# Kernel optimization log

Measured on AMD Instinct MI355X. Metric: run time of the kernel, lower is better.

The kernel has to match this reference:

```python
import jax, jax.numpy as jnp
import numpy as np

NUM_HEADS = 12
HEAD_SIZE = 64
HIDDEN = NUM_HEADS * HEAD_SIZE  # 768
ONE_SIDED_WINDOW = 256          # attention_window 512 // 2
NEG = -10000.0


def setup_inputs() -> dict:
    key = jax.random.key(0)
    ks = jax.random.split(key, 16)
    B, W, E, H = 1, 2048, 128, HIDDEN
    std = 0.02
    def lin(kw, kb):
        return (jax.random.normal(kw, (H, H), jnp.float32) * std,
                jax.random.normal(kb, (H,), jnp.float32) * std)
    q_w, q_b = lin(ks[0], ks[1])
    k_w, k_b = lin(ks[2], ks[3])
    v_w, v_b = lin(ks[4], ks[5])
    w2e_w, w2e_b = lin(ks[6], ks[7])
    e2w_w, e2w_b = lin(ks[8], ks[9])
    e2e_w, e2e_b = lin(ks[10], ks[11])
    return {
        "word_hidden_states": jax.random.normal(ks[12], (B, W, H), jnp.float32),
        "entity_hidden_states": jax.random.normal(ks[13], (B, E, H), jnp.float32),
        "attention_mask": jnp.zeros((B, 1, 1, W + E), jnp.float32),
        "q_w": q_w, "q_b": q_b, "k_w": k_w, "k_b": k_b, "v_w": v_w, "v_b": v_b,
        "w2e_w": w2e_w, "w2e_b": w2e_b, "e2w_w": e2w_w, "e2w_b": e2w_b,
        "e2e_w": e2e_w, "e2e_b": e2e_b,
    }


def reference(word_hidden_states, entity_hidden_states, attention_mask,
              q_w, q_b, k_w, k_b, v_w, v_b,
              w2e_w, w2e_b, e2w_w, e2w_b, e2e_w, e2e_b):
    B, W, H = word_hidden_states.shape
    E = entity_hidden_states.shape[1]
    S = W + E

    def heads(x):  # [B, L, H] -> [B, nh, L, hd]
        return x.reshape(B, -1, NUM_HEADS, HEAD_SIZE).transpose(0, 2, 1, 3)

    concat = jnp.concatenate([word_hidden_states, entity_hidden_states], axis=1)
    k = heads(concat @ k_w + k_b)          # [B, nh, S, hd]
    v = heads(concat @ v_w + v_b)
    q_w2w = heads(word_hidden_states @ q_w + q_b)
    q_w2e = heads(word_hidden_states @ w2e_w + w2e_b)
    q_e2w = heads(entity_hidden_states @ e2w_w + e2w_b)
    q_e2e = heads(entity_hidden_states @ e2e_w + e2e_b)

    k_word, k_ent = k[:, :, :W], k[:, :, W:]

    # --- w2w: Longformer sliding-window QK^T, then _conversion to a dense
    # [B, nh, W, W] matrix with out-of-band entries set to -10000. ---
    w2w = jnp.einsum('bhid,bhjd->bhij', q_w2w, k_word)  # [B, nh, W, W]
    idx = jnp.arange(W)
    in_band = jnp.abs(idx[:, None] - idx[None, :]) <= ONE_SIDED_WINDOW  # [W, W]
    # diagonal mask: float_mask[j] (-10000 where attention_mask != 0) added
    # within the band (broadcast over heads / query positions)
    mask_words = attention_mask[:, 0, 0, :W]                # [B, W]
    float_mask = jnp.where(mask_words != 0.0, NEG, 0.0)     # [B, W]
    w2w = w2w + float_mask[:, None, None, :]
    # _conversion: out-of-band -> -10000; also exact zeros -> -10000 (source quirk)
    w2w = jnp.where(in_band[None, None] & (w2w != 0.0), w2w, NEG)

    # --- entity-aware dense blocks ---
    w2e = jnp.einsum('bhid,bhjd->bhij', q_w2e, k_ent)    # [B, nh, W, E]
    e2w = jnp.einsum('bhid,bhjd->bhij', q_e2w, k_word)   # [B, nh, E, W]
    e2e = jnp.einsum('bhid,bhjd->bhij', q_e2e, k_ent)    # [B, nh, E, E]

    word_scores = jnp.concatenate([w2w, w2e], axis=3)    # [B, nh, W, S]
    ent_scores = jnp.concatenate([e2w, e2e], axis=3)     # [B, nh, E, S]
    scores = jnp.concatenate([word_scores, ent_scores], axis=2)  # [B, nh, S, S]

    scores = scores / jnp.sqrt(jnp.float32(HEAD_SIZE)) + attention_mask
    probs = jax.nn.softmax(scores, axis=-1)

    ctx = jnp.einsum('bhij,bhjd->bhid', probs, v)        # [B, nh, S, hd]
    ctx = ctx.transpose(0, 2, 1, 3).reshape(B, S, H)
    return ctx[:, :W, :], ctx[:, W:, :]
```

## Files before the change

kernel.cpp:

```cpp
#include <hip/hip_runtime.h>

typedef __bf16 bf16x8 __attribute__((ext_vector_type(8)));
typedef unsigned short u16x8 __attribute__((ext_vector_type(8)));
typedef u16x8 u16x8_a __attribute__((may_alias));
typedef unsigned int u32x2 __attribute__((ext_vector_type(2)));
typedef u32x2 u32x2_a __attribute__((may_alias));
typedef unsigned int u32x4 __attribute__((ext_vector_type(4)));
typedef u32x4 u32x4_a __attribute__((may_alias));
typedef float f32x4 __attribute__((ext_vector_type(4)));
typedef float f32x16 __attribute__((ext_vector_type(16)));

#define LOG2E 1.4426950408889634f
#define NEGV  -10000.0f

__device__ __forceinline__ unsigned int cvtpk(float lo, float hi){
  unsigned int r;
  asm("v_cvt_pk_bf16_f32 %0, %1, %2" : "=v"(r) : "v"(lo), "v"(hi));
  return r;
}
__device__ __forceinline__ bf16x8 ldb(const unsigned short* p){
  return __builtin_bit_cast(bf16x8, *(const u16x8_a*)p);
}
__device__ __forceinline__ bf16x8 mkfrag(unsigned a, unsigned b, unsigned c, unsigned d){
  u32x4 v = {a,b,c,d};
  return __builtin_bit_cast(bf16x8, v);
}
__device__ __forceinline__ void gload16(const unsigned short* g, unsigned short* l){
  __builtin_amdgcn_global_load_lds(
    (const __attribute__((address_space(1))) void*)g,
    (__attribute__((address_space(3))) void*)l, 16, 0, 0);
}

__global__ __launch_bounds__(256) void prep(
    const float* __restrict__ w0, const float* __restrict__ w1,
    const float* __restrict__ w2, const float* __restrict__ w3,
    const float* __restrict__ w4, const float* __restrict__ w5,
    const float* __restrict__ word, const float* __restrict__ ent,
    const float* __restrict__ am,
    unsigned short* __restrict__ outT, unsigned short* __restrict__ Abf,
    float* __restrict__ amT, float* __restrict__ negT)
{
  int z = blockIdx.z, tid = threadIdx.x;
  if (z == 6){
    size_t id = (size_t)blockIdx.y*24 + blockIdx.x;
    size_t e = (id*256 + tid)*8;
    const size_t WE = (size_t)2048*768;
    const float* s = (e < WE) ? (word + e) : (ent + (e - WE));
    float4 a = *(const float4*)s;
    float4 b = *(const float4*)(s+4);
    u32x4 v = {cvtpk(a.x,a.y), cvtpk(a.z,a.w), cvtpk(b.x,b.y), cvtpk(b.z,b.w)};
    *(u32x4_a*)(Abf + e) = v;
    return;
  }
  if (z == 7){
    if (blockIdx.y != 0 || blockIdx.x >= 9) return;
    int j = blockIdx.x*256 + tid;
    if (j < 2176){
      float a = am[j];
      amT[j]  = a * LOG2E;
      negT[j] = (a != 0.f) ? NEGV : 0.f;
    }
    return;
  }
  if (blockIdx.y >= 24) return;
  const float* src;
  switch (z){
    case 0: src = w0; break; case 1: src = w1; break; case 2: src = w2; break;
    case 3: src = w3; break; case 4: src = w4; break; default: src = w5; break;
  }
  unsigned short* dst = outT + (size_t)z * 589824;
  __shared__ float tile[32][33];
  int tx = tid & 31, ty = tid >> 5;
  int x0 = blockIdx.x*32, y0 = blockIdx.y*32;
  #pragma unroll
  for (int i=0;i<32;i+=8) tile[ty+i][tx] = src[(size_t)(y0+ty+i)*768 + x0+tx];
  __syncthreads();
  #pragma unroll
  for (int i=0;i<32;i+=16){
    unsigned int u = cvtpk(tile[tx][ty+i], tile[tx][ty+i+8]);
    dst[(size_t)(x0+ty+i)*768 + y0+tx]   = (unsigned short)u;
    dst[(size_t)(x0+ty+i+8)*768 + y0+tx] = (unsigned short)(u>>16);
  }
}

__global__ __launch_bounds__(256) void gemm_proj(
    const unsigned short* __restrict__ Abf,
    const unsigned short* __restrict__ wT,
    const float* __restrict__ bK, const float* __restrict__ bV,
    const float* __restrict__ bQ, const float* __restrict__ bWE,
    const float* __restrict__ bEW, const float* __restrict__ bEE,
    unsigned short* __restrict__ oK, unsigned short* __restrict__ VbT,
    unsigned short* __restrict__ oQ, unsigned short* __restrict__ oWE,
    unsigned short* __restrict__ oEW, unsigned short* __restrict__ oEE)
{
  int mt = blockIdx.x, ntile = blockIdx.y;
  int g, mg;
  if      (mt < 17){ g=0; mg=mt;    }
  else if (mt < 34){ g=1; mg=mt-17; }
  else if (mt < 50){ g=2; mg=mt-34; }
  else if (mt < 66){ g=3; mg=mt-50; }
  else if (mt < 67){ g=4; mg=0;     }
  else             { g=5; mg=0;     }
  int m0 = mg*128;
  const unsigned short* A = Abf + (size_t)((g>=4 ? 2048 : 0) + m0)*768;
  const unsigned short* B = wT + (size_t)g*589824;
  const float* bias; unsigned short* out;
  switch (g){
    case 0: bias=bK;  out=oK;  break;
    case 1: bias=bV;  out=0;   break;
    case 2: bias=bQ;  out=oQ;  break;
    case 3: bias=bWE; out=oWE; break;
    case 4: bias=bEW; out=oEW; break;
    default:bias=bEE; out=oEE; break;
  }
  int n0 = ntile*128;

  __shared__ __align__(16) unsigned short a_s[128*32];
  __shared__ __align__(16) unsigned short b_s[128*32];

  int tid  = threadIdx.x;
  int w    = tid>>6, lane = tid&63, quad = lane>>4, lr = lane&15;
  int wm   = (w&1)*64, wn = (w>>1)*64;

  f32x4 acc[4][4];
  #pragma unroll
  for (int i=0;i<4;i++) for (int j=0;j<4;j++) for (int r=0;r<4;r++) acc[i][j][r]=0.f;

  int srow = lane>>2;
  int scol = (lane&3)*8;
  const unsigned short* gA0 = A + (size_t)(w*32 + srow)*768 + scol;
  const unsigned short* gA1 = gA0 + (size_t)16*768;
  const unsigned short* gB0 = B + (size_t)(n0 + w*32 + srow)*768 + scol;
  const unsigned short* gB1 = gB0 + (size_t)16*768;
  unsigned short* lA0 = a_s + w*32*32;
  unsigned short* lA1 = lA0 + 16*32;
  unsigned short* lB0 = b_s + w*32*32;
  unsigned short* lB1 = lB0 + 16*32;

  for (int k0=0; k0<768; k0+=32){
    __syncthreads();
    gload16(gA0 + k0, lA0);
    gload16(gA1 + k0, lA1);
    gload16(gB0 + k0, lB0);
    gload16(gB1 + k0, lB1);
    __syncthreads();
    bf16x8 af[4], bfr[4];
    #pragma unroll
    for (int i=0;i<4;i++) af[i]  = ldb(a_s + (wm+i*16+lr)*32 + quad*8);
    #pragma unroll
    for (int j=0;j<4;j++) bfr[j] = ldb(b_s + (wn+j*16+lr)*32 + quad*8);
    #pragma unroll
    for (int i=0;i<4;i++)
      #pragma unroll
      for (int j=0;j<4;j++)
        acc[i][j] = __builtin_amdgcn_mfma_f32_16x16x32_bf16(af[i], bfr[j], acc[i][j], 0,0,0);
  }
  if (g == 1){
    #pragma unroll
    for (int j=0;j<4;j++){
      int col = n0 + wn + j*16 + lr;
      float bb = bias[col];
      #pragma unroll
      for (int i=0;i<4;i++){
        int rowb = m0 + wm + i*16 + quad*4;
        u32x2 uv = {cvtpk(acc[i][j][0]+bb, acc[i][j][1]+bb),
                    cvtpk(acc[i][j][2]+bb, acc[i][j][3]+bb)};
        *(u32x2_a*)(VbT + (size_t)col*2176 + rowb) = uv;
      }
    }
  } else {
    out += (size_t)m0*768;
    #pragma unroll
    for (int j=0;j<4;j++){
      int col = n0 + wn + j*16 + lr;
      float bb = bias[col];
      #pragma unroll
      for (int i=0;i<4;i++){
        int rowb = wm + i*16 + quad*4;
        unsigned int u01 = cvtpk(acc[i][j][0]+bb, acc[i][j][1]+bb);
        unsigned int u23 = cvtpk(acc[i][j][2]+bb, acc[i][j][3]+bb);
        out[(size_t)(rowb+0)*768 + col] = (unsigned short)u01;
        out[(size_t)(rowb+1)*768 + col] = (unsigned short)(u01>>16);
        out[(size_t)(rowb+2)*768 + col] = (unsigned short)u23;
        out[(size_t)(rowb+3)*768 + col] = (unsigned short)(u23>>16);
      }
    }
  }
}

__global__ __launch_bounds__(256, 4) void attn_split(
  const unsigned short* __restrict__ Kb,  const unsigned short* __restrict__ VbT,
  const unsigned short* __restrict__ Qw,  const unsigned short* __restrict__ Qwe,
  const unsigned short* __restrict__ Qew, const unsigned short* __restrict__ Qee,
  const float* __restrict__ amT, const float* __restrict__ negT,
  float* __restrict__ outw, float* __restrict__ pO, float* __restrict__ pML)
{
  int lin = blockIdx.x + 80*blockIdx.y;
  int wid = (lin & 7)*120 + (lin >> 3);
  int bx = wid % 80;
  int h  = wid / 80;

  int tid = threadIdx.x, w = tid>>6, lane = tid&63;
  int l31 = lane & 31, hi = lane >> 5;
  int hi8 = hi*8, hi4 = hi*4;
  bool isword = bx < 64;
  int qrb, eg=0, eq=0;
  const unsigned short *Qa, *Qb;
  if (isword){ qrb = bx*32; Qa=Qw;  Qb=Qwe; }
  else       { int e = bx-64; eg = e>>2; eq = e&3; qrb = eg*32; Qa=Qew; Qb=Qee; }
  int hofs = h*64;

  __shared__ float part[4][64][35];

  float m = -1e30f, l = 0.f;
  f32x16 o0, o1;
  #pragma unroll
  for (int r=0;r<16;r++){ o0[r] = 0.f; o1[r] = 0.f; }

  int lo, nw, start, end;
  if (isword){
    lo = qrb - 256; if (lo < 0) lo = 0;
    int hiq = qrb + 288; if (hiq > 2048) hiq = 2048;
    nw = (hiq - lo) >> 5;
    start = w; end = nw + 4;
  } else {
    lo = 0; nw = 64;
    start = eq*17 + w; end = eq*17 + 17;
  }
  int iq = qrb + l31;
  int end1 = (nw < end) ? nw : end;
  int c1   = start + ((nw - start + 3) & ~3);

#define AITER(J0, QF0, QF1, QF2, QF3, BAND) do { \
    int j0 = (J0); \
    const unsigned short* kp = Kb + (size_t)(j0+l31)*768 + hofs + hi8; \
    bf16x8 ka0 = ldb(kp), ka1 = ldb(kp+16), ka2 = ldb(kp+32), ka3 = ldb(kp+48); \
    float4 aT0 = *(const float4*)(amT + j0 + hi4); \
    float4 aT1 = *(const float4*)(amT + j0 + 8  + hi4); \
    float4 aT2 = *(const float4*)(amT + j0 + 16 + hi4); \
    float4 aT3 = *(const float4*)(amT + j0 + 24 + hi4); \
    f32x16 s; \
    _Pragma("unroll") \
    for (int r=0;r<16;r++) s[r] = 0.f; \
    __builtin_amdgcn_s_setprio(1); \
    s = __builtin_amdgcn_mfma_f32_32x32x16_bf16(ka0, QF0, s, 0,0,0); \
    s = __builtin_amdgcn_mfma_f32_32x32x16_bf16(ka1, QF1, s, 0,0,0); \
    s = __builtin_amdgcn_mfma_f32_32x32x16_bf16(ka2, QF2, s, 0,0,0); \
    s = __builtin_amdgcn_mfma_f32_32x32x16_bf16(ka3, QF3, s, 0,0,0); \
    __builtin_amdgcn_s_setprio(0); \
    const unsigned short* vp = VbT + (size_t)(hofs + l31)*2176 + j0 + hi8; \
    bf16x8 va00 = ldb(vp),           va01 = ldb(vp + 16); \
    bf16x8 va10 = ldb(vp + 32*2176), va11 = ldb(vp + 32*2176 + 16); \
    float sc[16]; \
    if (BAND){ \
      float4 nT0 = *(const float4*)(negT + j0 + hi4); \
      float4 nT1 = *(const float4*)(negT + j0 + 8  + hi4); \
      float4 nT2 = *(const float4*)(negT + j0 + 16 + hi4); \
      float4 nT3 = *(const float4*)(negT + j0 + 24 + hi4); \
      int djb = iq + 256 - (j0 + hi4); \
      _Pragma("unroll") \
      for (int e=0;e<4;e++){ \
        { float sv = s[e]    + nT0[e]; \
          bool ok = ((unsigned)(djb - e)      <= 512u) && (sv != 0.f); \
          sc[e]    = (ok ? sv : NEGV) * (LOG2E*0.125f) + aT0[e]; } \
        { float sv = s[4+e]  + nT1[e]; \
          bool ok = ((unsigned)(djb - 8 - e)  <= 512u) && (sv != 0.f); \
          sc[4+e]  = (ok ? sv : NEGV) * (LOG2E*0.125f) + aT1[e]; } \
        { float sv = s[8+e]  + nT2[e]; \
          bool ok = ((unsigned)(djb - 16 - e) <= 512u) && (sv != 0.f); \
          sc[8+e]  = (ok ? sv : NEGV) * (LOG2E*0.125f) + aT2[e]; } \
        { float sv = s[12+e] + nT3[e]; \
          bool ok = ((unsigned)(djb - 24 - e) <= 512u) && (sv != 0.f); \
          sc[12+e] = (ok ? sv : NEGV) * (LOG2E*0.125f) + aT3[e]; } \
      } \
    } else { \
      _Pragma("unroll") \
      for (int e=0;e<4;e++){ \
        sc[e]    = s[e]    * (LOG2E*0.125f) + aT0[e]; \
        sc[4+e]  = s[4+e]  * (LOG2E*0.125f) + aT1[e]; \
        sc[8+e]  = s[8+e]  * (LOG2E*0.125f) + aT2[e]; \
        sc[12+e] = s[12+e] * (LOG2E*0.125f) + aT3[e]; \
      } \
    } \
    float mx = sc[0]; \
    _Pragma("unroll") \
    for (int r=1;r<16;r++) mx = fmaxf(mx, sc[r]); \
    mx = fmaxf(mx, __shfl_xor(mx, 32)); \
    float mn; \
    if (__all(mx <= m)){ \
      mn = m; \
    } else { \
      mn = fmaxf(m, mx); \
      float alpha = exp2f(m - mn); \
      m = mn; \
      l *= alpha; \
      _Pragma("unroll") \
      for (int r=0;r<16;r++){ o0[r] *= alpha; o1[r] *= alpha; } \
    } \
    float p[16]; \
    _Pragma("unroll") \
    for (int r=0;r<16;r++) p[r] = exp2f(sc[r]-mn); \
    float rs = ((p[0]+p[1])+(p[2]+p[3])) + ((p[4]+p[5])+(p[6]+p[7])) \
             + ((p[8]+p[9])+(p[10]+p[11])) + ((p[12]+p[13])+(p[14]+p[15])); \
    rs += __shfl_xor(rs, 32); \
    l += rs; \
    unsigned pk0 = cvtpk(p[0], p[1]),  pk1 = cvtpk(p[2], p[3]); \
    unsigned pk2 = cvtpk(p[4], p[5]),  pk3 = cvtpk(p[6], p[7]); \
    unsigned pk4 = cvtpk(p[8], p[9]),  pk5 = cvtpk(p[10], p[11]); \
    unsigned pk6 = cvtpk(p[12], p[13]),pk7 = cvtpk(p[14], p[15]); \
    bool hib = hi != 0; \
    unsigned t0 = hib ? pk0 : pk2; \
    unsigned t1 = hib ? pk1 : pk3; \
    unsigned t2 = hib ? pk4 : pk6; \
    unsigned t3 = hib ? pk5 : pk7; \
    unsigned r0 = (unsigned)__shfl_xor((int)t0, 32); \
    unsigned r1 = (unsigned)__shfl_xor((int)t1, 32); \
    unsigned r2 = (unsigned)__shfl_xor((int)t2, 32); \
    unsigned r3 = (unsigned)__shfl_xor((int)t3, 32); \
    bf16x8 pf1 = hib ? mkfrag(r0, r1, pk2, pk3) : mkfrag(pk0, pk1, r0, r1); \
    bf16x8 pf2 = hib ? mkfrag(r2, r3, pk6, pk7) : mkfrag(pk4, pk5, r2, r3); \
    __builtin_amdgcn_s_setprio(1); \
    o0 = __builtin_amdgcn_mfma_f32_32x32x16_bf16(va00, pf1, o0, 0,0,0); \
    o0 = __builtin_amdgcn_mfma_f32_32x32x16_bf16(va01, pf2, o0, 0,0,0); \
    o1 = __builtin_amdgcn_mfma_f32_32x32x16_bf16(va10, pf1, o1, 0,0,0); \
    o1 = __builtin_amdgcn_mfma_f32_32x32x16_bf16(va11, pf2, o1, 0,0,0); \
    __builtin_amdgcn_s_setprio(0); \
  } while(0)

  {
    const unsigned short* qr = Qa + (size_t)(qrb+l31)*768 + hofs + hi8;
    bf16x8 qa0 = ldb(qr), qa1 = ldb(qr+16), qa2 = ldb(qr+32), qa3 = ldb(qr+48);
    for (int c = start; c < end1; c += 4)
      AITER(lo + c*32, qa0, qa1, qa2, qa3, isword);
  }
  __builtin_amdgcn_sched_barrier(0);
  if (c1 < end){
    const unsigned short* qr = Qb + (size_t)(qrb+l31)*768 + hofs + hi8;
    bf16x8 qb0 = ldb(qr), qb1 = ldb(qr+16), qb2 = ldb(qr+32), qb3 = ldb(qr+48);
    for (int c = c1; c < end; c += 4)
      AITER(2048 + (c-nw)*32, qb0, qb1, qb2, qb3, false);
  }
#undef AITER

  {
    float* my = &part[w][lane][0];
    my[0] = m; my[1] = l;
    #pragma unroll
    for (int r=0;r<16;r++){ my[2+r] = o0[r]; my[18+r] = o1[r]; }
  }
  __syncthreads();

  float mm[4], ll[4], e4[4];
  #pragma unroll
  for (int p=0;p<4;p++){ mm[p] = part[p][lane][0]; ll[p] = part[p][lane][1]; }
  float M = fmaxf(fmaxf(mm[0],mm[1]), fmaxf(mm[2],mm[3]));
  #pragma unroll
  for (int p=0;p<4;p++) e4[p] = exp2f(mm[p]-M);
  float L = ll[0]*e4[0] + ll[1]*e4[1] + ll[2]*e4[2] + ll[3]*e4[3];

  float mo0[4], mo1[4];
  #pragma unroll
  for (int k=0;k<4;k++){
    float a0 = 0.f, a1 = 0.f;
    #pragma unroll
    for (int p=0;p<4;p++){
      a0 += part[p][lane][2  + w*4 + k] * e4[p];
      a1 += part[p][lane][18 + w*4 + k] * e4[p];
    }
    mo0[k] = a0; mo1[k] = a1;
  }

  if (isword){
    float rinv = 1.f / L;
    float4 s0 = {mo0[0]*rinv, mo0[1]*rinv, mo0[2]*rinv, mo0[3]*rinv};
    float4 s1 = {mo1[0]*rinv, mo1[1]*rinv, mo1[2]*rinv, mo1[3]*rinv};
    float* ob = outw + (size_t)(qrb+l31)*768 + hofs + w*8 + hi4;
    *(float4*)(ob)      = s0;
    *(float4*)(ob + 32) = s1;
  } else {
    int idx = (eg*4 + eq)*12 + h;
    float* po = pO + (size_t)idx*2048 + l31*64 + w*8 + hi4;
    float4 s0 = {mo0[0], mo0[1], mo0[2], mo0[3]};
    float4 s1 = {mo1[0], mo1[1], mo1[2], mo1[3]};
    *(float4*)(po)      = s0;
    *(float4*)(po + 32) = s1;
    if (w == 0 && lane < 32){
      float* pml = pML + (size_t)idx*64;
      pml[lane*2]     = M;
      pml[lane*2 + 1] = L;
    }
  }
}

__global__ __launch_bounds__(256) void merge_ent(
    const float* __restrict__ pO, const float* __restrict__ pML,
    float* __restrict__ oute)
{
  int b = blockIdx.x;
  int eg = b/12, h = b%12;
  int tid = threadIdx.x;
  int row = tid>>3, cg = (tid&7)*8;
  float mq[4], lq[4];
  #pragma unroll
  for (int q=0;q<4;q++){
    int idx = (eg*4 + q)*12 + h;
    mq[q] = pML[(size_t)idx*64 + row*2];
    lq[q] = pML[(size_t)idx*64 + row*2 + 1];
  }
  float M = fmaxf(fmaxf(mq[0],mq[1]), fmaxf(mq[2],mq[3]));
  float L = 0.f, eqv[4];
  #pragma unroll
  for (int q=0;q<4;q++){ eqv[q] = exp2f(mq[q]-M); L += lq[q]*eqv[q]; }
  float rl = 1.f/L;
  float4 a0 = {0,0,0,0}, a1 = {0,0,0,0};
  #pragma unroll
  for (int q=0;q<4;q++){
    int idx = (eg*4 + q)*12 + h;
    const float* src = pO + (size_t)idx*2048 + row*64 + cg;
    float4 x = *(const float4*)(src);
    float4 y = *(const float4*)(src + 4);
    a0.x += x.x*eqv[q]; a0.y += x.y*eqv[q]; a0.z += x.z*eqv[q]; a0.w += x.w*eqv[q];
    a1.x += y.x*eqv[q]; a1.y += y.y*eqv[q]; a1.z += y.z*eqv[q]; a1.w += y.w*eqv[q];
  }
  a0.x*=rl; a0.y*=rl; a0.z*=rl; a0.w*=rl;
  a1.x*=rl; a1.y*=rl; a1.z*=rl; a1.w*=rl;
  float* dst = oute + (size_t)(eg*32+row)*768 + h*64 + cg;
  *(float4*)(dst)   = a0;
  *(float4*)(dst+4) = a1;
}

extern "C" void kernel_launch(void* const* d_in, const int* in_sizes, int n_in,
                              void* d_out, int out_size, void* d_ws, size_t ws_size,
                              hipStream_t stream) {
  const float* word  = (const float*)d_in[0];
  const float* ent   = (const float*)d_in[1];
  const float* am    = (const float*)d_in[2];
  const float* q_w   = (const float*)d_in[3];
  const float* q_b   = (const float*)d_in[4];
  const float* k_w   = (const float*)d_in[5];
  const float* k_b   = (const float*)d_in[6];
  const float* v_w   = (const float*)d_in[7];
  const float* v_b   = (const float*)d_in[8];
  const float* w2e_w = (const float*)d_in[9];
  const float* w2e_b = (const float*)d_in[10];
  const float* e2w_w = (const float*)d_in[11];
  const float* e2w_b = (const float*)d_in[12];
  const float* e2e_w = (const float*)d_in[13];
  const float* e2e_b = (const float*)d_in[14];

  unsigned short* ws  = (unsigned short*)d_ws;
  unsigned short* wT  = ws;
  unsigned short* Kb  = wT  + (size_t)6*589824;
  unsigned short* Tb  = Kb  + (size_t)2176*768;
  unsigned short* Qw  = Tb  + (size_t)2176*768;
  unsigned short* Qwe = Qw  + (size_t)2048*768;
  unsigned short* Qew = Qwe + (size_t)2048*768;
  unsigned short* Qee = Qew + (size_t)128*768;
  unsigned short* VbT = Qee + (size_t)128*768;
  unsigned short* Abf = VbT + (size_t)768*2176;

  float* amT  = (float*)Tb;
  float* negT = amT + 2176;

  float* pO  = (float*)wT;
  float* pML = pO + (size_t)192*2048;

  float* outw = (float*)d_out;
  float* oute = outw + (size_t)2048*768;

  hipLaunchKernelGGL(prep, dim3(24,34,8), dim3(256), 0, stream,
                     k_w, v_w, q_w, w2e_w, e2w_w, e2e_w, word, ent, am,
                     wT, Abf, amT, negT);
  hipLaunchKernelGGL(gemm_proj, dim3(68,6), dim3(256), 0, stream,
                     Abf, wT, k_b, v_b, q_b, w2e_b, e2w_b, e2e_b,
                     Kb, VbT, Qw, Qwe, Qew, Qee);
  hipLaunchKernelGGL(attn_split, dim3(80,12), dim3(256), 0, stream,
                     Kb, VbT, Qw, Qwe, Qew, Qee, amT, negT, outw, pO, pML);
  hipLaunchKernelGGL(merge_ent, dim3(48), dim3(256), 0, stream,
                     pO, pML, oute);
}
```

Measured before the change: 154.2 us.

## Double-buffer K fragments in registers and relax attention kernel launch bounds

The attention loop now loads the next tile's K fragments into a second register set before it computes the current tile, alternating between two buffers. This hides global-load latency behind the MFMA and softmax work. The entity tail loop becomes a single iteration because it can run at most once, and the sched_barrier is dropped. The min-blocks-per-CU hint of 4 is removed so the compiler can use more registers for the extra buffers, at the risk of lower occupancy.

```diff
diff --git a/kernel.cpp b/kernel.cpp
--- a/kernel.cpp
+++ b/kernel.cpp
@@ -188,7 +188,7 @@
   }
 }
 
-__global__ __launch_bounds__(256, 4) void attn_split(
+__global__ __launch_bounds__(256) void attn_split(
   const unsigned short* __restrict__ Kb,  const unsigned short* __restrict__ VbT,
   const unsigned short* __restrict__ Qw,  const unsigned short* __restrict__ Qwe,
   const unsigned short* __restrict__ Qew, const unsigned short* __restrict__ Qee,
@@ -217,47 +217,45 @@
   #pragma unroll
   for (int r=0;r<16;r++){ o0[r] = 0.f; o1[r] = 0.f; }
 
-  int lo, nw, start, end;
+  int lo, b, s1, endT;
   if (isword){
     lo = qrb - 256; if (lo < 0) lo = 0;
     int hiq = qrb + 288; if (hiq > 2048) hiq = 2048;
-    nw = (hiq - lo) >> 5;
-    start = w; end = nw + 4;
+    b = (hiq - lo) >> 5;
+    s1 = w; endT = b + 4;
   } else {
-    lo = 0; nw = 64;
-    start = eq*17 + w; end = eq*17 + 17;
-  }
+    lo = 0; b = 64;
+    s1 = eq*17 + w; endT = eq*17 + 17;
+  }
+  int e1 = (b < endT) ? b : endT;
+  int c2 = s1 + ((e1 - s1 + 3) & ~3);
   int iq = qrb + l31;
-  int end1 = (nw < end) ? nw : end;
-  int c1   = start + ((nw - start + 3) & ~3);
-
-#define AITER(J0, QF0, QF1, QF2, QF3, BAND) do { \
-    int j0 = (J0); \
-    const unsigned short* kp = Kb + (size_t)(j0+l31)*768 + hofs + hi8; \
-    bf16x8 ka0 = ldb(kp), ka1 = ldb(kp+16), ka2 = ldb(kp+32), ka3 = ldb(kp+48); \
-    float4 aT0 = *(const float4*)(amT + j0 + hi4); \
-    float4 aT1 = *(const float4*)(amT + j0 + 8  + hi4); \
-    float4 aT2 = *(const float4*)(amT + j0 + 16 + hi4); \
-    float4 aT3 = *(const float4*)(amT + j0 + 24 + hi4); \
+
+#define BODY(J0, K0, K1, K2, K3, BAND) do { \
+    int jb = (J0); \
+    float4 aT0 = *(const float4*)(amT + jb + hi4); \
+    float4 aT1 = *(const float4*)(amT + jb + 8  + hi4); \
+    float4 aT2 = *(const float4*)(amT + jb + 16 + hi4); \
+    float4 aT3 = *(const float4*)(amT + jb + 24 + hi4); \
     f32x16 s; \
     _Pragma("unroll") \
     for (int r=0;r<16;r++) s[r] = 0.f; \
     __builtin_amdgcn_s_setprio(1); \
-    s = __builtin_amdgcn_mfma_f32_32x32x16_bf16(ka0, QF0, s, 0,0,0); \
-    s = __builtin_amdgcn_mfma_f32_32x32x16_bf16(ka1, QF1, s, 0,0,0); \
-    s = __builtin_amdgcn_mfma_f32_32x32x16_bf16(ka2, QF2, s, 0,0,0); \
-    s = __builtin_amdgcn_mfma_f32_32x32x16_bf16(ka3, QF3, s, 0,0,0); \
+    s = __builtin_amdgcn_mfma_f32_32x32x16_bf16(K0, qf0, s, 0,0,0); \
+    s = __builtin_amdgcn_mfma_f32_32x32x16_bf16(K1, qf1, s, 0,0,0); \
+    s = __builtin_amdgcn_mfma_f32_32x32x16_bf16(K2, qf2, s, 0,0,0); \
+    s = __builtin_amdgcn_mfma_f32_32x32x16_bf16(K3, qf3, s, 0,0,0); \
     __builtin_amdgcn_s_setprio(0); \
-    const unsigned short* vp = VbT + (size_t)(hofs + l31)*2176 + j0 + hi8; \
+    const unsigned short* vp = VbT + (size_t)(hofs + l31)*2176 + jb + hi8; \
     bf16x8 va00 = ldb(vp),           va01 = ldb(vp + 16); \
     bf16x8 va10 = ldb(vp + 32*2176), va11 = ldb(vp + 32*2176 + 16); \
     float sc[16]; \
     if (BAND){ \
-      float4 nT0 = *(const float4*)(negT + j0 + hi4); \
-      float4 nT1 = *(const float4*)(negT + j0 + 8  + hi4); \
-      float4 nT2 = *(const float4*)(negT + j0 + 16 + hi4); \
-      float4 nT3 = *(const float4*)(negT + j0 + 24 + hi4); \
-      int djb = iq + 256 - (j0 + hi4); \
+      float4 nT0 = *(const float4*)(negT + jb + hi4); \
+      float4 nT1 = *(const float4*)(negT + jb + 8  + hi4); \
+      float4 nT2 = *(const float4*)(negT + jb + 16 + hi4); \
+      float4 nT3 = *(const float4*)(negT + jb + 24 + hi4); \
+      int djb = iq + 256 - (jb + hi4); \
       _Pragma("unroll") \
       for (int e=0;e<4;e++){ \
         { float sv = s[e]    + nT0[e]; \
@@ -327,20 +325,42 @@
     __builtin_amdgcn_s_setprio(0); \
   } while(0)
 
+#define LOADK(K0, K1, K2, K3, J0) do { \
+    const unsigned short* kp_ = Kb + (size_t)((J0)+l31)*768 + hofs + hi8; \
+    K0 = ldb(kp_); K1 = ldb(kp_+16); K2 = ldb(kp_+32); K3 = ldb(kp_+48); \
+  } while(0)
+
   {
     const unsigned short* qr = Qa + (size_t)(qrb+l31)*768 + hofs + hi8;
-    bf16x8 qa0 = ldb(qr), qa1 = ldb(qr+16), qa2 = ldb(qr+32), qa3 = ldb(qr+48);
-    for (int c = start; c < end1; c += 4)
-      AITER(lo + c*32, qa0, qa1, qa2, qa3, isword);
-  }
-  __builtin_amdgcn_sched_barrier(0);
-  if (c1 < end){
+    bf16x8 qf0 = ldb(qr), qf1 = ldb(qr+16), qf2 = ldb(qr+32), qf3 = ldb(qr+48);
+    bool band = isword;
+    bf16x8 kA0,kA1,kA2,kA3, kB0,kB1,kB2,kB3;
+    int c = s1;
+    LOADK(kA0,kA1,kA2,kA3, lo + c*32);
+    while (true){
+      int cn = c + 4;
+      bool mb = cn < e1;
+      if (mb) LOADK(kB0,kB1,kB2,kB3, lo + cn*32);
+      BODY(lo + c*32, kA0,kA1,kA2,kA3, band);
+      if (!mb) break;
+      int cnn = cn + 4;
+      bool ma = cnn < e1;
+      if (ma) LOADK(kA0,kA1,kA2,kA3, lo + cnn*32);
+      BODY(lo + cn*32, kB0,kB1,kB2,kB3, band);
+      if (!ma) break;
+      c = cnn;
+    }
+  }
+  if (c2 < endT){
     const unsigned short* qr = Qb + (size_t)(qrb+l31)*768 + hofs + hi8;
-    bf16x8 qb0 = ldb(qr), qb1 = ldb(qr+16), qb2 = ldb(qr+32), qb3 = ldb(qr+48);
-    for (int c = c1; c < end; c += 4)
-      AITER(2048 + (c-nw)*32, qb0, qb1, qb2, qb3, false);
-  }
-#undef AITER
+    bf16x8 qf0 = ldb(qr), qf1 = ldb(qr+16), qf2 = ldb(qr+32), qf3 = ldb(qr+48);
+    int j2base = 2048 + (c2 - b)*32;
+    bf16x8 kC0,kC1,kC2,kC3;
+    LOADK(kC0,kC1,kC2,kC3, j2base);
+    BODY(j2base, kC0,kC1,kC2,kC3, false);
+  }
+#undef BODY
+#undef LOADK
 
   {
     float* my = &part[w][lane][0];
@@ -373,17 +393,17 @@
   if (isword){
     float rinv = 1.f / L;
     float4 s0 = {mo0[0]*rinv, mo0[1]*rinv, mo0[2]*rinv, mo0[3]*rinv};
-    float4 s1 = {mo1[0]*rinv, mo1[1]*rinv, mo1[2]*rinv, mo1[3]*rinv};
+    float4 s1v = {mo1[0]*rinv, mo1[1]*rinv, mo1[2]*rinv, mo1[3]*rinv};
     float* ob = outw + (size_t)(qrb+l31)*768 + hofs + w*8 + hi4;
     *(float4*)(ob)      = s0;
-    *(float4*)(ob + 32) = s1;
+    *(float4*)(ob + 32) = s1v;
   } else {
     int idx = (eg*4 + eq)*12 + h;
     float* po = pO + (size_t)idx*2048 + l31*64 + w*8 + hi4;
     float4 s0 = {mo0[0], mo0[1], mo0[2], mo0[3]};
-    float4 s1 = {mo1[0], mo1[1], mo1[2], mo1[3]};
+    float4 s1v = {mo1[0], mo1[1], mo1[2], mo1[3]};
     *(float4*)(po)      = s0;
-    *(float4*)(po + 32) = s1;
+    *(float4*)(po + 32) = s1v;
     if (w == 0 && lane < 32){
       float* pml = pML + (size_t)idx*64;
       pml[lane*2]     = M;
```

Result: no change. 151.3 us (-1.8%).
